# Kernel optimization log

Hardware: AMD Instinct MI355X
Metric: run time of the kernel (lower is better)

## Reference

```python
import jax, jax.numpy as jnp
import numpy as np

EMBED_DIM = 1024
NUM_HEADS = 16
CONTEXT = 250
MAX_PERIOD = 10000.0
HEAD_DIM = EMBED_DIM // NUM_HEADS


def setup_inputs() -> dict:
    key = jax.random.key(0)
    k1, k2, k3 = jax.random.split(key, 3)
    B, T = 2, 2048
    query = jax.random.normal(k1, (B, T, EMBED_DIM), jnp.float32)
    in_proj_w = jax.random.normal(k2, (3 * EMBED_DIM, EMBED_DIM), jnp.float32) * (EMBED_DIM ** -0.5)
    out_proj_w = jax.random.normal(k3, (EMBED_DIM, EMBED_DIM), jnp.float32) * (EMBED_DIM ** -0.5)
    return {"query": query, "in_proj_w": in_proj_w, "out_proj_w": out_proj_w}


def _apply_rope(q, k):
    # q, k: [B, H, T, D]; Mimi/Moshi-style interleaved-pair rotary embedding
    B, H, T, D = q.shape
    ds = jnp.arange(D // 2, dtype=jnp.float32)
    freqs = jnp.exp(ds * (-np.log(MAX_PERIOD) * 2.0 / D))  # [D/2]
    ts = jnp.arange(T, dtype=jnp.float32)
    ang = ts[:, None] * freqs[None, :]  # [T, D/2]
    cos = jnp.cos(ang)
    sin = jnp.sin(ang)

    def rot(x):
        xr = x.reshape(B, H, T, D // 2, 2)
        xa, xb = xr[..., 0], xr[..., 1]
        ya = xa * cos - xb * sin
        yb = xa * sin + xb * cos
        return jnp.stack([ya, yb], axis=-1).reshape(B, H, T, D)

    return rot(q), rot(k)


def reference(query, in_proj_w, out_proj_w):
    B, T, E = query.shape
    H, D = NUM_HEADS, HEAD_DIM
    # fused QKV projection (no bias)
    proj = query @ in_proj_w.T  # [B, T, 3E]
    qkv = proj.reshape(B, T, 3, H, D)
    q = jnp.transpose(qkv[:, :, 0], (0, 2, 1, 3))  # [B, H, T, D]
    k = jnp.transpose(qkv[:, :, 1], (0, 2, 1, 3))
    v = jnp.transpose(qkv[:, :, 2], (0, 2, 1, 3))
    q, k = _apply_rope(q, k)
    # causal sliding-window mask: attend iff 0 <= (t_q - t_k) < CONTEXT
    pos = jnp.arange(T)
    delta = pos[:, None] - pos[None, :]  # [T, T]
    mask = (delta >= 0) & (delta < CONTEXT)
    scores = jnp.einsum('bhtd,bhsd->bhts', q, k) * (D ** -0.5)
    scores = jnp.where(mask[None, None, :, :], scores, jnp.finfo(scores.dtype).min)
    attn = jax.nn.softmax(scores, axis=-1)
    x = jnp.einsum('bhts,bhsd->bhtd', attn, v)  # [B, H, T, D]
    x = jnp.transpose(x, (0, 2, 1, 3)).reshape(B, T, E)
    return x @ out_proj_w.T
```

## Files before the change

kernel.cpp:

```cpp
#include <hip/hip_runtime.h>

#define TT 2048
#define EMB 1024
#define NH 16
#define HD 64
#define CTX 250

typedef __attribute__((ext_vector_type(4))) float f32x4;
typedef __attribute__((ext_vector_type(8))) short s16x8;
typedef __attribute__((ext_vector_type(4))) short s16x4;

#define LDS_PTR(p) ((__attribute__((address_space(3))) void*)(p))
#define GLB_PTR(p) ((const __attribute__((address_space(1))) void*)(p))

__device__ __forceinline__ short f2bf(float f) {
  union { float f; unsigned u; } v; v.f = f;
  unsigned r = v.u + 0x7fffu + ((v.u >> 16) & 1u);
  return (short)(r >> 16);
}
__device__ __forceinline__ float bf2f(unsigned short u) {
  union { unsigned u; float f; } v; v.u = ((unsigned)u) << 16;
  return v.f;
}

__global__ void cvt_all(const float* __restrict__ q, const float* __restrict__ wi,
                        const float* __restrict__ wo, short* __restrict__ qo,
                        short* __restrict__ wio, short* __restrict__ woo) {
  int i = blockIdx.x * blockDim.x + threadIdx.x;
  const float* src; short* dst; int off;
  if (i < 1048576)      { src = q;  dst = qo;  off = i; }
  else if (i < 1835008) { src = wi; dst = wio; off = i - 1048576; }
  else                  { src = wo; dst = woo; off = i - 1835008; }
  float4 v = reinterpret_cast<const float4*>(src)[off];
  s16x4 o; o[0] = f2bf(v.x); o[1] = f2bf(v.y); o[2] = f2bf(v.z); o[3] = f2bf(v.w);
  *reinterpret_cast<s16x4*>(dst + off * 4) = o;
}

template<int BM, bool BF16OUT>
__global__ __launch_bounds__(256) void gemm_lds(const short* __restrict__ A,
                                                const short* __restrict__ W,
                                                void* __restrict__ Cv, int N, int K) {
  constexpr int BK = 32;
  constexpr int MFR = BM / 32;
  __shared__ __align__(16) short As[BM * BK];
  __shared__ __align__(16) short Bs[128 * BK];
  const int lane = threadIdx.x & 63;
  const int wid  = threadIdx.x >> 6;
  const int lr = lane & 15, lg = lane >> 4;
  const int rblk = blockIdx.y * BM;
  const int cblk = blockIdx.x * 128;
  const int wrow = (wid >> 1) * (BM / 2);
  const int wcol = (wid & 1) * 64;
  const int srow = lane >> 2;
  const int scol = (lane & 3) * 8;
  f32x4 acc[MFR][4] = {};

  for (int kk = 0; kk < K; kk += BK) {
#pragma unroll
    for (int j = 0; j < BM / 64; j++) {
      int seg = wid * (BM / 64) + j;
      const short* g = A + (size_t)(rblk + seg * 16 + srow) * K + kk + scol;
      __builtin_amdgcn_global_load_lds(GLB_PTR(g), LDS_PTR(&As[seg * 512]), 16, 0, 0);
    }
#pragma unroll
    for (int j = 0; j < 2; j++) {
      int seg = wid * 2 + j;
      const short* g = W + (size_t)(cblk + seg * 16 + srow) * K + kk + scol;
      __builtin_amdgcn_global_load_lds(GLB_PTR(g), LDS_PTR(&Bs[seg * 512]), 16, 0, 0);
    }
    __syncthreads();
    s16x8 af[MFR], bfr[4];
#pragma unroll
    for (int m = 0; m < MFR; m++)
      af[m] = *reinterpret_cast<const s16x8*>(&As[(wrow + m * 16 + lr) * BK + lg * 8]);
#pragma unroll
    for (int n = 0; n < 4; n++)
      bfr[n] = *reinterpret_cast<const s16x8*>(&Bs[(wcol + n * 16 + lr) * BK + lg * 8]);
#pragma unroll
    for (int m = 0; m < MFR; m++)
#pragma unroll
      for (int n = 0; n < 4; n++)
        acc[m][n] = __builtin_amdgcn_mfma_f32_16x16x32_bf16(af[m], bfr[n], acc[m][n], 0, 0, 0);
    __syncthreads();
  }
#pragma unroll
  for (int m = 0; m < MFR; m++)
#pragma unroll
    for (int n = 0; n < 4; n++)
#pragma unroll
      for (int r = 0; r < 4; r++) {
        int row = rblk + wrow + m * 16 + lg * 4 + r;
        int col = cblk + wcol + n * 16 + lr;
        float val = acc[m][n][r];
        if constexpr (BF16OUT) ((short*)Cv)[(size_t)row * N + col] = f2bf(val);
        else                   ((float*)Cv)[(size_t)row * N + col] = val;
      }
}

__global__ __launch_bounds__(256) void rope_v2(const short* __restrict__ proj,
                                               short* __restrict__ Qb,
                                               short* __restrict__ Kb,
                                               short* __restrict__ Vt) {
  int tid = threadIdx.x;
  int t0 = blockIdx.x * 64;
  int bh = blockIdx.y;
  int b = bh >> 4, h = bh & 15;
  __shared__ short vtile[64 * 66];
  int i = tid & 31;
  int trow = tid >> 5;
  float freq = __expf(-(float)i * 0.2878231366f);
#pragma unroll
  for (int it = 0; it < 8; ++it) {
    int tl = it * 8 + trow;
    int t = t0 + tl;
    int pbase = (b * TT + t) * 3 * EMB + h * HD + 2 * i;
    unsigned q01 = *reinterpret_cast<const unsigned*>(proj + pbase);
    unsigned k01 = *reinterpret_cast<const unsigned*>(proj + pbase + EMB);
    unsigned v01 = *reinterpret_cast<const unsigned*>(proj + pbase + 2 * EMB);
    float qa = bf2f((unsigned short)(q01 & 0xffff)), qb_ = bf2f((unsigned short)(q01 >> 16));
    float ka = bf2f((unsigned short)(k01 & 0xffff)), kb_ = bf2f((unsigned short)(k01 >> 16));
    float ang = (float)t * freq;
    float s, c;
    sincosf(ang, &s, &c);
    int obase = (bh * TT + t) * HD + 2 * i;
    unsigned qo = ((unsigned)(unsigned short)f2bf(qa * s + qb_ * c) << 16) |
                  (unsigned short)f2bf(qa * c - qb_ * s);
    unsigned ko = ((unsigned)(unsigned short)f2bf(ka * s + kb_ * c) << 16) |
                  (unsigned short)f2bf(ka * c - kb_ * s);
    *reinterpret_cast<unsigned*>(Qb + obase) = qo;
    *reinterpret_cast<unsigned*>(Kb + obase) = ko;
    *reinterpret_cast<unsigned*>(&vtile[tl * 66 + 2 * i]) = v01;
  }
  __syncthreads();
  int d = tid >> 2, toff = (tid & 3) * 16;
  s16x8 o0, o1;
#pragma unroll
  for (int j = 0; j < 8; ++j) {
    o0[j] = vtile[(toff + j) * 66 + d];
    o1[j] = vtile[(toff + 8 + j) * 66 + d];
  }
  size_t vb = (size_t)(bh * HD + d) * TT + t0 + toff;
  *reinterpret_cast<s16x8*>(Vt + vb) = o0;
  *reinterpret_cast<s16x8*>(Vt + vb + 8) = o1;
}

__global__ __launch_bounds__(256) void attn_v4(const short* __restrict__ Qb,
                                               const short* __restrict__ Kb,
                                               const short* __restrict__ Vt,
                                               short* __restrict__ Xout) {
  int tid = threadIdx.x;
  int lane = tid & 63;
  int w = tid >> 6;
  int lr = lane & 15, lg = lane >> 4;
  int id = blockIdx.x;
  int xcd = id & 7;
  int sub = id >> 3;
  int bh = xcd * 4 + (sub >> 5);
  int tblk = (sub & 31) * 64;
  int t0 = tblk + w * 16;
  int b = bh >> 4, h = bh & 15;
  const short* Qp = Qb + bh * TT * HD;
  const char* Kp = (const char*)(Kb + bh * TT * HD);
  const char* Vtp = (const char*)(Vt + bh * HD * TT);
  __shared__ __align__(16) short Ks[32 * 64];
  __shared__ __align__(16) short Vs[64 * 32];
  __shared__ __align__(16) short p_lds[4][16][40];
  s16x8 qf[2];
#pragma unroll
  for (int d2 = 0; d2 < 2; d2++)
    qf[d2] = *reinterpret_cast<const s16x8*>(Qp + (t0 + lr) * HD + d2 * 32 + lg * 8);
  s16x8 ones;
#pragma unroll
  for (int j = 0; j < 8; j++) ones[j] = (short)0x3F80;
  f32x4 of[4] = {};
  f32x4 ofl = {};
  int lo = tblk - (CTX - 1); if (lo < 0) lo = 0;
  int kt_lo = lo & ~31;
  int kt_hi = (tblk + 63) & ~31;
  int krow = w * 8 + (lane >> 3);
  int kcb  = ((lane & 7) * 16) ^ ((krow & 7) << 4);
  int vd   = w * 16 + (lane >> 2);
  int vcb  = ((lane & 3) * 16) ^ (((vd >> 1) & 3) << 4);
  char* ksdst = (char*)Ks + w * 1024 + lane * 16;
  char* vsdst = (char*)Vs + w * 1024 + lane * 16;
  for (int kt = kt_lo; kt <= kt_hi; kt += 32) {
    __builtin_amdgcn_global_load_lds(GLB_PTR(Kp + (kt + krow) * 128 + kcb),
                                     LDS_PTR(ksdst), 16, 0, 0);
    __builtin_amdgcn_global_load_lds(GLB_PTR(Vtp + vd * (TT * 2) + kt * 2 + vcb),
                                     LDS_PTR(vsdst), 16, 0, 0);
    __syncthreads();
    if (kt <= t0 + 15 && kt + 31 >= t0 - (CTX - 1)) {
      f32x4 s2[2];
#pragma unroll
      for (int hh = 0; hh < 2; hh++) {
        int row = hh * 16 + lr;
        f32x4 sa = {};
#pragma unroll
        for (int d2 = 0; d2 < 2; d2++) {
          int cb = (d2 * 64 + lg * 16) ^ ((row & 7) << 4);
          s16x8 kf = *reinterpret_cast<const s16x8*>((const char*)Ks + row * 128 + cb);
          sa = __builtin_amdgcn_mfma_f32_16x16x32_bf16(qf[d2], kf, sa, 0, 0, 0);
        }
        s2[hh] = sa;
      }
#pragma unroll
      for (int r = 0; r < 4; r++) {
        int row = t0 + lg * 4 + r;
#pragma unroll
        for (int hh = 0; hh < 2; hh++) {
          int col = kt + hh * 16 + lr;
          int dl = row - col;
          bool vdm = (dl >= 0) && (dl < CTX);
          float pv = vdm ? __expf(s2[hh][r] * 0.125f) : 0.0f;
          p_lds[w][lg * 4 + r][hh * 16 + lr] = f2bf(pv);
        }
      }
      s16x8 pa = *reinterpret_cast<const s16x8*>(&p_lds[w][lr][lg * 8]);
#pragma unroll
      for (int n = 0; n < 4; n++) {
        int d = n * 16 + lr;
        int cb = (lg * 16) ^ (((d >> 1) & 3) << 4);
        s16x8 vf = *reinterpret_cast<const s16x8*>((const char*)Vs + d * 64 + cb);
        of[n] = __builtin_amdgcn_mfma_f32_16x16x32_bf16(pa, vf, of[n], 0, 0, 0);
      }
      ofl = __builtin_amdgcn_mfma_f32_16x16x32_bf16(pa, ones, ofl, 0, 0, 0);
    }
    __syncthreads();
  }
#pragma unroll
  for (int r = 0; r < 4; r++) {
    float inv = 1.0f / ofl[r];
    int row = t0 + lg * 4 + r;
#pragma unroll
    for (int n = 0; n < 4; n++)
      Xout[(b * TT + row) * EMB + h * HD + n * 16 + lr] = f2bf(of[n][r] * inv);
  }
}

extern "C" void kernel_launch(void* const* d_in, const int* in_sizes, int n_in,
                              void* d_out, int out_size, void* d_ws, size_t ws_size,
                              hipStream_t stream) {
  const float* query = (const float*)d_in[0];
  const float* w_in  = (const float*)d_in[1];
  const float* w_out = (const float*)d_in[2];
  char* ws = (char*)d_ws;
  short* qbf   = (short*)(ws + 0);
  short* wibf  = (short*)(ws + 8388608);
  short* wobf  = (short*)(ws + 14680064);
  short* proj  = (short*)(ws + 16777216);
  short* attnx = (short*)(ws + 16777216);
  short* Qb    = (short*)(ws + 41943040);
  short* Kb    = (short*)(ws + 50331648);
  short* Vt    = (short*)(ws + 58720256);

  cvt_all<<<8192, 256, 0, stream>>>(query, w_in, w_out, qbf, wibf, wobf);
  gemm_lds<128, true><<<dim3(24, 32), 256, 0, stream>>>(qbf, wibf, (void*)proj, 3072, 1024);
  rope_v2<<<dim3(32, 32), 256, 0, stream>>>(proj, Qb, Kb, Vt);
  attn_v4<<<1024, 256, 0, stream>>>(Qb, Kb, Vt, attnx);
  gemm_lds<64, false><<<dim3(8, 64), 256, 0, stream>>>(attnx, wobf, d_out, 1024, 1024);
}
```

Baseline: 98.22 us.

## Swizzle GEMM LDS layout and remap blocks per XCD for L2 locality

The GEMM kernel now XOR-swizzles the 16-byte chunks it writes into LDS and reads back, so the MFMA fragment loads avoid LDS bank conflicts. It also switches to a 1D grid and remaps block indices so that the blocks landing on each of the 8 XCDs (assigned round-robin) cover a contiguous 2D sub-tile of the output, which improves L2 reuse of A and W tiles. The mapping assumes specific grid factorizations (LX, LY) that must exactly tile the output. Getting those wrong would leave tiles uncomputed.

```diff
diff --git a/kernel.cpp b/kernel.cpp
--- a/kernel.cpp
+++ b/kernel.cpp
@@ -36,8 +36,8 @@
   *reinterpret_cast<s16x4*>(dst + off * 4) = o;
 }
 
-template<int BM, bool BF16OUT>
-__global__ __launch_bounds__(256) void gemm_lds(const short* __restrict__ A,
+template<int BM, int LX, int LY, bool BF16OUT>
+__global__ __launch_bounds__(256) void gemm_swz(const short* __restrict__ A,
                                                 const short* __restrict__ W,
                                                 void* __restrict__ Cv, int N, int K) {
   constexpr int BK = 32;
@@ -47,35 +47,42 @@
   const int lane = threadIdx.x & 63;
   const int wid  = threadIdx.x >> 6;
   const int lr = lane & 15, lg = lane >> 4;
-  const int rblk = blockIdx.y * BM;
-  const int cblk = blockIdx.x * 128;
-  const int wrow = (wid >> 1) * (BM / 2);
-  const int wcol = (wid & 1) * 64;
-  const int srow = lane >> 2;
-  const int scol = (lane & 3) * 8;
+  const int xcd = blockIdx.x & 7;
+  const int sub = blockIdx.x >> 3;
+  const int bx = (sub % LX) + LX * (xcd & 1);
+  const int by = (sub / LX) + LY * (xcd >> 1);
+  const int rblk = by * BM;
+  const int cblk = bx * 128;
+  const int wrow16 = (wid >> 1) * MFR;
+  const int wcol16 = (wid & 1) * 4;
+  const int lrow = lane >> 2;
+  const int fst  = (lrow & 3) ^ ((lrow >> 2) & 3);
+  const int schunk = ((lane & 3) ^ fst) * 8;
+  const int frd = (lr & 3) ^ ((lr >> 2) & 3);
+  const int rd_off = lr * 32 + ((lg ^ frd) * 8);
   f32x4 acc[MFR][4] = {};
 
   for (int kk = 0; kk < K; kk += BK) {
 #pragma unroll
     for (int j = 0; j < BM / 64; j++) {
       int seg = wid * (BM / 64) + j;
-      const short* g = A + (size_t)(rblk + seg * 16 + srow) * K + kk + scol;
+      const short* g = A + (size_t)(rblk + seg * 16 + lrow) * K + kk + schunk;
       __builtin_amdgcn_global_load_lds(GLB_PTR(g), LDS_PTR(&As[seg * 512]), 16, 0, 0);
     }
 #pragma unroll
     for (int j = 0; j < 2; j++) {
       int seg = wid * 2 + j;
-      const short* g = W + (size_t)(cblk + seg * 16 + srow) * K + kk + scol;
+      const short* g = W + (size_t)(cblk + seg * 16 + lrow) * K + kk + schunk;
       __builtin_amdgcn_global_load_lds(GLB_PTR(g), LDS_PTR(&Bs[seg * 512]), 16, 0, 0);
     }
     __syncthreads();
     s16x8 af[MFR], bfr[4];
 #pragma unroll
     for (int m = 0; m < MFR; m++)
-      af[m] = *reinterpret_cast<const s16x8*>(&As[(wrow + m * 16 + lr) * BK + lg * 8]);
+      af[m] = *reinterpret_cast<const s16x8*>(&As[(wrow16 + m) * 512 + rd_off]);
 #pragma unroll
     for (int n = 0; n < 4; n++)
-      bfr[n] = *reinterpret_cast<const s16x8*>(&Bs[(wcol + n * 16 + lr) * BK + lg * 8]);
+      bfr[n] = *reinterpret_cast<const s16x8*>(&Bs[(wcol16 + n) * 512 + rd_off]);
 #pragma unroll
     for (int m = 0; m < MFR; m++)
 #pragma unroll
@@ -89,8 +96,8 @@
     for (int n = 0; n < 4; n++)
 #pragma unroll
       for (int r = 0; r < 4; r++) {
-        int row = rblk + wrow + m * 16 + lg * 4 + r;
-        int col = cblk + wcol + n * 16 + lr;
+        int row = rblk + (wrow16 + m) * 16 + lg * 4 + r;
+        int col = cblk + (wcol16 + n) * 16 + lr;
         float val = acc[m][n][r];
         if constexpr (BF16OUT) ((short*)Cv)[(size_t)row * N + col] = f2bf(val);
         else                   ((float*)Cv)[(size_t)row * N + col] = val;
@@ -254,8 +261,8 @@
   short* Vt    = (short*)(ws + 58720256);
 
   cvt_all<<<8192, 256, 0, stream>>>(query, w_in, w_out, qbf, wibf, wobf);
-  gemm_lds<128, true><<<dim3(24, 32), 256, 0, stream>>>(qbf, wibf, (void*)proj, 3072, 1024);
+  gemm_swz<128, 12, 8, true><<<768, 256, 0, stream>>>(qbf, wibf, (void*)proj, 3072, 1024);
   rope_v2<<<dim3(32, 32), 256, 0, stream>>>(proj, Qb, Kb, Vt);
   attn_v4<<<1024, 256, 0, stream>>>(Qb, Kb, Vt, attnx);
-  gemm_lds<64, false><<<dim3(8, 64), 256, 0, stream>>>(attnx, wobf, d_out, 1024, 1024);
-}
+  gemm_swz<64, 4, 16, false><<<512, 256, 0, stream>>>(attnx, wobf, d_out, 1024, 1024);
+}
```

Result: no change. 97.27 us (-1.0%).

## Replace QKV GEMM with 256x256 8-phase pipelined kernel and swizzle output GEMM

Applied to the files above, without the earlier changes.

The QKV projection GEMM now uses a new 512-thread kernel with 256x256 tiles, a 128-wide K step, and 128KB of double-buffered LDS. Global-to-LDS loads are split into half-tile phases interleaved with MFMA groups, with explicit waitcnt, barriers, setprio and XOR-swizzled LDS addressing, so memory traffic overlaps compute and bank conflicts drop. The block index is also remapped across XCDs for L2 locality. The output-projection GEMM keeps its old body but gets an XCD-aware block swizzle. The cost is one block per CU with heavy register use and hand-tuned sync that relies on exact vmcnt counts.

```diff
diff --git a/kernel.cpp b/kernel.cpp
--- a/kernel.cpp
+++ b/kernel.cpp
@@ -36,8 +36,139 @@
   *reinterpret_cast<s16x4*>(dst + off * 4) = o;
 }
 
-template<int BM, bool BF16OUT>
-__global__ __launch_bounds__(256) void gemm_lds(const short* __restrict__ A,
+__global__ __launch_bounds__(512, 1) void gemm_8ph(const short* __restrict__ A,
+                                                   const short* __restrict__ W,
+                                                   short* __restrict__ C, int N, int K) {
+  __shared__ short lds8[65536];
+  char* ldsc = (char*)lds8;
+  const int tid = threadIdx.x, lane = tid & 63, wid = tid >> 6;
+  const int lr = lane & 15, lg = lane >> 4;
+  const int wm = wid >> 2, wn = wid & 3;
+  const int swz = (blockIdx.x & 7) * 24 + (blockIdx.x >> 3);
+  const int rblk = (swz / 12) << 8;
+  const int cblk = (swz % 12) << 8;
+  const int srowL = lane >> 2;
+  const int schunkL = ((lane & 3) ^ ((lane >> 5) << 1)) * 8;
+  const int innerRd = (lr * 64 + lg * 16) ^ ((lr & 8) << 2);
+  f32x4 acc[8][4] = {};
+
+#define ST_HALF(mat, tile, h)                                                      \
+  { const short* Gp = (mat) ? W : A;                                               \
+    const int blkoff = (mat) ? cblk : rblk;                                        \
+    _Pragma("unroll") for (int j = 0; j < 2; ++j) {                                \
+      int u = wid * 2 + j;                                                         \
+      const short* g = Gp + (size_t)(blkoff + (h) * 128 + (u & 7) * 16 + srowL) * K \
+                       + (tile) * 64 + (u >> 3) * 32 + schunkL;                    \
+      __builtin_amdgcn_global_load_lds(GLB_PTR(g),                                 \
+          LDS_PTR(ldsc + (mat) * 65536 + ((tile) & 1) * 32768 + (h) * 16384        \
+                  + u * 1024), 16, 0, 0);                                          \
+    } }
+
+#define LD_A(dbuf, m, kk) \
+  (*reinterpret_cast<const s16x8*>(ldsc + (dbuf) * 32768 + wm * 16384 + ((kk) * 8 + (m)) * 1024 + innerRd))
+#define LD_B(dbuf, n, kk) \
+  (*reinterpret_cast<const s16x8*>(ldsc + 65536 + (dbuf) * 32768 + (wn >> 1) * 16384 + ((kk) * 8 + (wn & 1) * 4 + (n)) * 1024 + innerRd))
+
+#define BARRIER __builtin_amdgcn_s_barrier()
+#define LGKM0 { asm volatile("s_waitcnt lgkmcnt(0)" ::: "memory"); __builtin_amdgcn_sched_barrier(0); }
+#define MFMA16(MB, NB, AF, BF)                                                     \
+  { __builtin_amdgcn_s_setprio(1);                                                 \
+    _Pragma("unroll") for (int m = 0; m < 4; ++m)                                  \
+      _Pragma("unroll") for (int n = 0; n < 2; ++n)                                \
+        _Pragma("unroll") for (int kk = 0; kk < 2; ++kk)                           \
+          acc[(MB) + m][(NB) + n] = __builtin_amdgcn_mfma_f32_16x16x32_bf16(       \
+              AF[m][kk], BF[n][kk], acc[(MB) + m][(NB) + n], 0, 0, 0);             \
+    __builtin_amdgcn_s_setprio(0); }
+
+  ST_HALF(0, 0, 0) ST_HALF(0, 0, 1) ST_HALF(1, 0, 0) ST_HALF(1, 0, 1)
+  ST_HALF(0, 1, 0) ST_HALF(0, 1, 1) ST_HALF(1, 1, 0) ST_HALF(1, 1, 1)
+  asm volatile("s_waitcnt vmcnt(8)" ::: "memory");
+  BARRIER;
+
+  const int NI = K >> 7;
+  for (int i = 0; i < NI; ++i) {
+    const int t0k = 2 * i, t1k = 2 * i + 1;
+    const bool stA1 = (i >= 1);
+    const bool stN  = (i < NI - 1);
+    s16x8 afr[4][2], bf0[2][2], bf1[2][2];
+
+#pragma unroll
+    for (int m = 0; m < 4; ++m) { afr[m][0] = LD_A(0, m, 0); afr[m][1] = LD_A(0, m, 1); }
+#pragma unroll
+    for (int n = 0; n < 2; ++n) { bf0[n][0] = LD_B(0, n, 0); bf0[n][1] = LD_B(0, n, 1); }
+    if (stA1) ST_HALF(0, t1k, 0)
+    BARRIER; LGKM0;
+    MFMA16(0, 0, afr, bf0);
+    BARRIER;
+
+#pragma unroll
+    for (int n = 0; n < 2; ++n) { bf1[n][0] = LD_B(0, n + 2, 0); bf1[n][1] = LD_B(0, n + 2, 1); }
+    if (stA1) ST_HALF(0, t1k, 1)
+    BARRIER; LGKM0;
+    MFMA16(0, 2, afr, bf1);
+    BARRIER;
+
+#pragma unroll
+    for (int m = 0; m < 4; ++m) { afr[m][0] = LD_A(0, m + 4, 0); afr[m][1] = LD_A(0, m + 4, 1); }
+    if (stN) ST_HALF(1, t0k + 2, 0)
+    BARRIER; LGKM0;
+    MFMA16(4, 2, afr, bf1);
+    BARRIER;
+
+    if (stN) ST_HALF(1, t0k + 2, 1)
+    if (stN) { asm volatile("s_waitcnt vmcnt(4)" ::: "memory"); }
+    else     { asm volatile("s_waitcnt vmcnt(0)" ::: "memory"); }
+    BARRIER; __builtin_amdgcn_sched_barrier(0);
+    MFMA16(4, 0, afr, bf0);
+    BARRIER;
+
+#pragma unroll
+    for (int m = 0; m < 4; ++m) { afr[m][0] = LD_A(1, m, 0); afr[m][1] = LD_A(1, m, 1); }
+#pragma unroll
+    for (int n = 0; n < 2; ++n) { bf0[n][0] = LD_B(1, n, 0); bf0[n][1] = LD_B(1, n, 1); }
+    if (stN) ST_HALF(0, t0k + 2, 0)
+    BARRIER; LGKM0;
+    MFMA16(0, 0, afr, bf0);
+    BARRIER;
+
+#pragma unroll
+    for (int n = 0; n < 2; ++n) { bf1[n][0] = LD_B(1, n + 2, 0); bf1[n][1] = LD_B(1, n + 2, 1); }
+    if (stN) ST_HALF(0, t0k + 2, 1)
+    BARRIER; LGKM0;
+    MFMA16(0, 2, afr, bf1);
+    BARRIER;
+
+#pragma unroll
+    for (int m = 0; m < 4; ++m) { afr[m][0] = LD_A(1, m + 4, 0); afr[m][1] = LD_A(1, m + 4, 1); }
+    if (stN) ST_HALF(1, t1k + 2, 0)
+    BARRIER; LGKM0;
+    MFMA16(4, 2, afr, bf1);
+    BARRIER;
+
+    if (stN) ST_HALF(1, t1k + 2, 1)
+    if (stN) { asm volatile("s_waitcnt vmcnt(4)" ::: "memory"); }
+    BARRIER; __builtin_amdgcn_sched_barrier(0);
+    MFMA16(4, 0, afr, bf0);
+    BARRIER;
+  }
+#undef ST_HALF
+#undef LD_A
+#undef LD_B
+
+#pragma unroll
+  for (int mf = 0; mf < 8; ++mf)
+#pragma unroll
+    for (int nf = 0; nf < 4; ++nf)
+#pragma unroll
+      for (int r = 0; r < 4; ++r) {
+        int row = rblk + wm * 128 + mf * 16 + lg * 4 + r;
+        int col = cblk + wn * 64 + nf * 16 + lr;
+        C[(size_t)row * N + col] = f2bf(acc[mf][nf][r]);
+      }
+}
+
+template<int BM, int LX, int LY, bool BF16OUT>
+__global__ __launch_bounds__(256) void gemm_swz(const short* __restrict__ A,
                                                 const short* __restrict__ W,
                                                 void* __restrict__ Cv, int N, int K) {
   constexpr int BK = 32;
@@ -47,8 +178,12 @@
   const int lane = threadIdx.x & 63;
   const int wid  = threadIdx.x >> 6;
   const int lr = lane & 15, lg = lane >> 4;
-  const int rblk = blockIdx.y * BM;
-  const int cblk = blockIdx.x * 128;
+  const int xcd = blockIdx.x & 7;
+  const int sub = blockIdx.x >> 3;
+  const int bx = (sub % LX) + LX * (xcd & 1);
+  const int by = (sub / LX) + LY * (xcd >> 1);
+  const int rblk = by * BM;
+  const int cblk = bx * 128;
   const int wrow = (wid >> 1) * (BM / 2);
   const int wcol = (wid & 1) * 64;
   const int srow = lane >> 2;
@@ -254,8 +389,8 @@
   short* Vt    = (short*)(ws + 58720256);
 
   cvt_all<<<8192, 256, 0, stream>>>(query, w_in, w_out, qbf, wibf, wobf);
-  gemm_lds<128, true><<<dim3(24, 32), 256, 0, stream>>>(qbf, wibf, (void*)proj, 3072, 1024);
+  gemm_8ph<<<192, 512, 0, stream>>>(qbf, wibf, proj, 3072, 1024);
   rope_v2<<<dim3(32, 32), 256, 0, stream>>>(proj, Qb, Kb, Vt);
   attn_v4<<<1024, 256, 0, stream>>>(Qb, Kb, Vt, attnx);
-  gemm_lds<64, false><<<dim3(8, 64), 256, 0, stream>>>(attnx, wobf, d_out, 1024, 1024);
-}
+  gemm_swz<64, 4, 16, false><<<512, 256, 0, stream>>>(attnx, wobf, d_out, 1024, 1024);
+}
```

New measurement: 93.45 us. 4.9% less time.
